# Kernel optimization log

Hardware: AMD Instinct MI355X
Metric: run time of the kernel (lower is better)

The kernel has to match this reference:

```python
import jax, jax.numpy as jnp
import numpy as np

MARGIN = 0.1
LAMBDA_EFFECT = 0.5

B, T_V, K, T_S = 32, 8192, 64, 128


def setup_inputs() -> dict:
    key = jax.random.key(0)
    k1, k2, k3, k4, k5 = jax.random.split(key, 5)
    pred_orig = jax.random.normal(k1, (B, T_V), dtype=jnp.float32)
    pred_intervened = jax.random.normal(k2, (K, B, T_V), dtype=jnp.float32)
    intervened_indices = jax.random.randint(k3, (K,), 0, T_S, dtype=jnp.int32)
    # GT alignment mask: sparse-ish binary alignment between frames and sentences
    gt_mask = jax.random.bernoulli(k4, 0.2, (B, T_V, T_S)).astype(jnp.int32)
    # prefix-valid video mask: valid length per batch in [T_V//2, T_V]
    lengths = jax.random.randint(k5, (B,), T_V // 2, T_V + 1, dtype=jnp.int32)
    mask_video = (jnp.arange(T_V, dtype=jnp.int32)[None, :] < lengths[:, None]).astype(jnp.int32)
    return {
        "pred_orig": pred_orig,
        "pred_intervened": pred_intervened,
        "intervened_indices": intervened_indices,
        "gt_mask": gt_mask,
        "mask_video": mask_video,
    }


def reference(pred_orig, pred_intervened, intervened_indices, gt_mask, mask_video):
    # pred_orig: [B,T], pred_intervened: [K,B,T], gt_mask: [B,T,S], mask_video: [B,T]
    prob_orig = jax.nn.sigmoid(pred_orig)                 # [B,T]
    prob_int = jax.nn.sigmoid(pred_intervened)            # [K,B,T]
    effect = jnp.abs(prob_orig[None, :, :] - prob_int)    # [K,B,T]

    valid = mask_video.astype(bool)                       # [B,T] (prefix mask == :T_v_valid slice)
    # gather intervened sentence columns: [B,T,K] -> [K,B,T]
    gt_sel = jnp.transpose(gt_mask[:, :, intervened_indices], (2, 0, 1))

    aligned = (gt_sel > 0) & valid[None]                  # [K,B,T]
    non_aligned = (gt_sel == 0) & valid[None]             # [K,B,T]

    cnt_a = aligned.sum(axis=-1)                          # [K,B]
    cnt_n = non_aligned.sum(axis=-1)                      # [K,B]

    ea = jnp.sum(effect * aligned, axis=-1) / jnp.maximum(cnt_a, 1)
    en = jnp.sum(effect * non_aligned, axis=-1) / jnp.maximum(cnt_n, 1)

    per_pair = jnp.where((cnt_a > 0) & (cnt_n > 0),
                         jax.nn.relu(MARGIN - (ea - en)),
                         jnp.zeros_like(ea))
    num_interventions = pred_orig.shape[0] * pred_intervened.shape[0]
    alignment_consistency = per_pair.sum() / max(num_interventions, 1)
    total_intervention_loss = alignment_consistency * LAMBDA_EFFECT
    return alignment_consistency, total_intervention_loss
```

## Files before the change

### kernel.cpp

```cpp
#include <hip/hip_runtime.h>
#include <cstdint>

#define BB 32
#define TV 8192
#define KK 64
#define TS 128
#define MARGIN_F 0.1f
#define LAMBDA_F 0.5f

static constexpr size_t WSA_OFF = 0;
static constexpr size_t WSV_OFF = (size_t)BB * TV * 8;
static constexpr size_t ACC_OFF = WSV_OFF + (size_t)BB * (TV / 64) * 8;

__global__ __launch_bounds__(256) void pack_kernel(
    const int* __restrict__ gt, const int* __restrict__ mv,
    const int* __restrict__ idx,
    unsigned long long* __restrict__ wsA, unsigned long long* __restrict__ wsV) {
  const int lane = threadIdx.x & 63;
  const int wave = blockIdx.x * 4 + (threadIdx.x >> 6);
  const int r0 = wave * 64;
  const int c = idx[lane];
  const int csel = c & 3, csh = c >> 2;

  const unsigned long long V = __ballot(mv[r0 + lane] != 0);
  if (lane == 0) wsV[r0 >> 6] = V;

  const int4* rowp = (const int4*)(gt + (size_t)r0 * TS);
#pragma unroll 2
  for (int ch = 0; ch < 32; ++ch) {
    int4 v = rowp[ch * 64 + lane];
    unsigned long long b0 = __ballot(v.x > 0);
    unsigned long long b1 = __ballot(v.y > 0);
    unsigned long long b2 = __ballot(v.z > 0);
    unsigned long long b3 = __ballot(v.w > 0);
    unsigned long long sel = (csel == 0) ? b0 : (csel == 1) ? b1 : (csel == 2) ? b2 : b3;
    int raw0 = (int)((sel >> csh) & 1ull);
    int raw1 = (int)((sel >> (32 + csh)) & 1ull);
    const int rlo = 2 * ch, rhi = 2 * ch + 1;
    const int v0 = (int)((V >> rlo) & 1ull);
    const int v1 = (int)((V >> rhi) & 1ull);
    unsigned long long A0 = __ballot(v0 & raw0);
    unsigned long long A1 = __ballot(v1 & raw1);
    if (lane == 0) {
      wsA[r0 + rlo] = A0;
      wsA[r0 + rhi] = A1;
    }
  }
}

__global__ __launch_bounds__(256) void main_kernel(
    const float* __restrict__ po, const float* __restrict__ pi,
    const unsigned long long* __restrict__ wsA,
    const unsigned long long* __restrict__ wsV, float* __restrict__ acc) {
  const int k = blockIdx.x & (KK - 1);
  const int b = blockIdx.x >> 6;
  const float* pik = pi + ((size_t)k * BB + b) * TV;
  const float* pob = po + (size_t)b * TV;
  const unsigned long long* Ab = wsA + (size_t)b * TV;
  const unsigned long long* Vb = wsV + (size_t)b * (TV / 64);

  float ea = 0.f, en = 0.f;
  int ca = 0, cn = 0;
  for (int t = threadIdx.x; t < TV; t += 256) {
    const float xo = pob[t];
    const float xi = pik[t];
    const unsigned long long A = Ab[t];
    const int valid = (int)((Vb[t >> 6] >> (t & 63)) & 1ull);
    const int ab = (int)((A >> k) & 1ull);
    const int nb = valid & (ab ^ 1);
    const float so = 1.f / (1.f + __expf(-xo));
    const float si = 1.f / (1.f + __expf(-xi));
    const float eff = fabsf(so - si);
    ea += ab ? eff : 0.f;
    en += nb ? eff : 0.f;
    ca += ab;
    cn += nb;
  }
#pragma unroll
  for (int off = 32; off > 0; off >>= 1) {
    ea += __shfl_down(ea, off);
    en += __shfl_down(en, off);
    ca += __shfl_down(ca, off);
    cn += __shfl_down(cn, off);
  }
  __shared__ float sea[4], sen[4];
  __shared__ int sca[4], scn[4];
  const int w = threadIdx.x >> 6;
  if ((threadIdx.x & 63) == 0) { sea[w] = ea; sen[w] = en; sca[w] = ca; scn[w] = cn; }
  __syncthreads();
  if (threadIdx.x == 0) {
    float EA = 0.f, EN = 0.f;
    int CA = 0, CN = 0;
#pragma unroll
    for (int i = 0; i < 4; ++i) { EA += sea[i]; EN += sen[i]; CA += sca[i]; CN += scn[i]; }
    float pp = 0.f;
    if (CA > 0 && CN > 0) {
      const float d = MARGIN_F - (EA / (float)CA - EN / (float)CN);
      pp = d > 0.f ? d : 0.f;
    }
    atomicAdd(acc, pp);
  }
}

__global__ void fin_kernel(const float* __restrict__ acc, float* __restrict__ out) {
  const float s = acc[0] * (1.0f / (float)(BB * KK));
  out[0] = s;
  out[1] = s * LAMBDA_F;
}

extern "C" void kernel_launch(void* const* d_in, const int* in_sizes, int n_in,
                              void* d_out, int out_size, void* d_ws, size_t ws_size,
                              hipStream_t stream) {
  const float* pred_orig = (const float*)d_in[0];
  const float* pred_int  = (const float*)d_in[1];
  const int*   idx       = (const int*)d_in[2];
  const int*   gt        = (const int*)d_in[3];
  const int*   mv        = (const int*)d_in[4];
  float* out = (float*)d_out;

  char* ws = (char*)d_ws;
  unsigned long long* wsA = (unsigned long long*)(ws + WSA_OFF);
  unsigned long long* wsV = (unsigned long long*)(ws + WSV_OFF);
  float* acc = (float*)(ws + ACC_OFF);

  hipMemsetAsync(acc, 0, sizeof(float), stream);
  pack_kernel<<<1024, 256, 0, stream>>>(gt, mv, idx, wsA, wsV);
  main_kernel<<<BB * KK, 256, 0, stream>>>(pred_orig, pred_int, wsA, wsV, acc);
  fin_kernel<<<1, 1, 0, stream>>>(acc, out);
}
```

Baseline: 280.0 us.

## Fuse mask packing and effect reduction into one row-tiled kernel with atomics

Merges the pack and main kernels so each wave packs the aligned bits for its 64 rows into LDS, then loops over all K interventions for those rows. The per-row workspace bitmask no longer makes a round trip through global memory, pred_orig sigmoid is computed once per row instead of K times, and one launch is removed. Non-aligned sums are derived as valid-minus-aligned in a small final kernel. The cost is many float atomics (three per wave per k, plus one per wave for the valid count) and strided access to pred_intervened across k.

```diff
diff --git a/kernel.cpp b/kernel.cpp
--- a/kernel.cpp
+++ b/kernel.cpp
@@ -8,22 +8,27 @@
 #define MARGIN_F 0.1f
 #define LAMBDA_F 0.5f
 
-static constexpr size_t WSA_OFF = 0;
-static constexpr size_t WSV_OFF = (size_t)BB * TV * 8;
-static constexpr size_t ACC_OFF = WSV_OFF + (size_t)BB * (TV / 64) * 8;
+static constexpr int KSTR = BB * TV;
 
-__global__ __launch_bounds__(256) void pack_kernel(
-    const int* __restrict__ gt, const int* __restrict__ mv,
-    const int* __restrict__ idx,
-    unsigned long long* __restrict__ wsA, unsigned long long* __restrict__ wsV) {
+
+__global__ __launch_bounds__(256) void fused_kernel(
+    const float* __restrict__ po, const float* __restrict__ pi,
+    const int* __restrict__ idx, const int* __restrict__ gt,
+    const int* __restrict__ mv,
+    float* __restrict__ gsa, float* __restrict__ gsv,
+    float* __restrict__ gca, float* __restrict__ gcv) {
   const int lane = threadIdx.x & 63;
-  const int wave = blockIdx.x * 4 + (threadIdx.x >> 6);
+  const int w = threadIdx.x >> 6;
+  const int wave = blockIdx.x * 4 + w;
   const int r0 = wave * 64;
+  const int b = r0 >> 13;
   const int c = idx[lane];
   const int csel = c & 3, csh = c >> 2;
 
+  __shared__ unsigned long long lA[256];
+  unsigned long long* A = lA + w * 64;
+
   const unsigned long long V = __ballot(mv[r0 + lane] != 0);
-  if (lane == 0) wsV[r0 >> 6] = V;
 
   const int4* rowp = (const int4*)(gt + (size_t)r0 * TS);
 #pragma unroll 2
@@ -41,71 +46,67 @@
     const int v1 = (int)((V >> rhi) & 1ull);
     unsigned long long A0 = __ballot(v0 & raw0);
     unsigned long long A1 = __ballot(v1 & raw1);
+    if (lane == 0) { A[rlo] = A0; A[rhi] = A1; }
+  }
+  __syncthreads();
+
+  const unsigned long long Am = A[lane];
+  const int vb = (int)((V >> lane) & 1ull);
+  const float xo = po[r0 + lane];
+  const float so = 1.f / (1.f + __expf(-xo));
+  const float* pik = pi + r0 + lane;
+
+  if (lane == 0) atomicAdd(&gcv[b], (float)__popcll(V));
+
+#pragma unroll 4
+  for (int k = 0; k < KK; ++k) {
+    const float xi = pik[(size_t)k * KSTR];
+    const float si = 1.f / (1.f + __expf(-xi));
+    const float eff = fabsf(so - si);
+    const int ab = (int)((Am >> k) & 1ull);
+    float sa = ab ? eff : 0.f;
+    float sv = vb ? eff : 0.f;
+#pragma unroll
+    for (int off = 32; off > 0; off >>= 1) {
+      sa += __shfl_down(sa, off);
+      sv += __shfl_down(sv, off);
+    }
+    const unsigned long long cab = __ballot(ab != 0);
     if (lane == 0) {
-      wsA[r0 + rlo] = A0;
-      wsA[r0 + rhi] = A1;
+      atomicAdd(&gsa[k * BB + b], sa);
+      atomicAdd(&gsv[k * BB + b], sv);
+      atomicAdd(&gca[k * BB + b], (float)__popcll(cab));
     }
   }
 }
 
-__global__ __launch_bounds__(256) void main_kernel(
-    const float* __restrict__ po, const float* __restrict__ pi,
-    const unsigned long long* __restrict__ wsA,
-    const unsigned long long* __restrict__ wsV, float* __restrict__ acc) {
-  const int k = blockIdx.x & (KK - 1);
-  const int b = blockIdx.x >> 6;
-  const float* pik = pi + ((size_t)k * BB + b) * TV;
-  const float* pob = po + (size_t)b * TV;
-  const unsigned long long* Ab = wsA + (size_t)b * TV;
-  const unsigned long long* Vb = wsV + (size_t)b * (TV / 64);
-
-  float ea = 0.f, en = 0.f;
-  int ca = 0, cn = 0;
-  for (int t = threadIdx.x; t < TV; t += 256) {
-    const float xo = pob[t];
-    const float xi = pik[t];
-    const unsigned long long A = Ab[t];
-    const int valid = (int)((Vb[t >> 6] >> (t & 63)) & 1ull);
-    const int ab = (int)((A >> k) & 1ull);
-    const int nb = valid & (ab ^ 1);
-    const float so = 1.f / (1.f + __expf(-xo));
-    const float si = 1.f / (1.f + __expf(-xi));
-    const float eff = fabsf(so - si);
-    ea += ab ? eff : 0.f;
-    en += nb ? eff : 0.f;
-    ca += ab;
-    cn += nb;
+__global__ __launch_bounds__(256) void fin_kernel(
+    const float* __restrict__ gsa, const float* __restrict__ gsv,
+    const float* __restrict__ gca, const float* __restrict__ gcv,
+    float* __restrict__ out) {
+  float s = 0.f;
+  for (int i = threadIdx.x; i < KK * BB; i += 256) {
+    const int b = i & (BB - 1);
+    const float ca = gca[i];
+    const float cn = gcv[b] - ca;
+    if (ca > 0.f && cn > 0.f) {
+      const float sa = gsa[i];
+      const float sv = gsv[i];
+      const float d = MARGIN_F - (sa / ca - (sv - sa) / cn);
+      s += d > 0.f ? d : 0.f;
+    }
   }
 #pragma unroll
-  for (int off = 32; off > 0; off >>= 1) {
-    ea += __shfl_down(ea, off);
-    en += __shfl_down(en, off);
-    ca += __shfl_down(ca, off);
-    cn += __shfl_down(cn, off);
-  }
-  __shared__ float sea[4], sen[4];
-  __shared__ int sca[4], scn[4];
-  const int w = threadIdx.x >> 6;
-  if ((threadIdx.x & 63) == 0) { sea[w] = ea; sen[w] = en; sca[w] = ca; scn[w] = cn; }
+  for (int off = 32; off > 0; off >>= 1) s += __shfl_down(s, off);
+  __shared__ float ws4[4];
+  if ((threadIdx.x & 63) == 0) ws4[threadIdx.x >> 6] = s;
   __syncthreads();
   if (threadIdx.x == 0) {
-    float EA = 0.f, EN = 0.f;
-    int CA = 0, CN = 0;
-#pragma unroll
-    for (int i = 0; i < 4; ++i) { EA += sea[i]; EN += sen[i]; CA += sca[i]; CN += scn[i]; }
-    float pp = 0.f;
-    if (CA > 0 && CN > 0) {
-      const float d = MARGIN_F - (EA / (float)CA - EN / (float)CN);
-      pp = d > 0.f ? d : 0.f;
-    }
-    atomicAdd(acc, pp);
+    const float S = ws4[0] + ws4[1] + ws4[2] + ws4[3];
+    const float ac = S * (1.0f / (float)(KK * BB));
+    out[0] = ac;
+    out[1] = ac * LAMBDA_F;
   }
-}
-
-__global__ void fin_kernel(const float* __restrict__ acc, float* __restrict__ out) {
-  const float s = acc[0] * (1.0f / (float)(BB * KK));
-  out[0] = s;
-  out[1] = s * LAMBDA_F;
 }
 
 extern "C" void kernel_launch(void* const* d_in, const int* in_sizes, int n_in,
@@ -118,13 +119,13 @@
   const int*   mv        = (const int*)d_in[4];
   float* out = (float*)d_out;
 
-  char* ws = (char*)d_ws;
-  unsigned long long* wsA = (unsigned long long*)(ws + WSA_OFF);
-  unsigned long long* wsV = (unsigned long long*)(ws + WSV_OFF);
-  float* acc = (float*)(ws + ACC_OFF);
+  float* gsa = (float*)d_ws;
+  float* gsv = gsa + KK * BB;
+  float* gca = gsv + KK * BB;
+  float* gcv = gca + KK * BB;
 
-  hipMemsetAsync(acc, 0, sizeof(float), stream);
-  pack_kernel<<<1024, 256, 0, stream>>>(gt, mv, idx, wsA, wsV);
-  main_kernel<<<BB * KK, 256, 0, stream>>>(pred_orig, pred_int, wsA, wsV, acc);
-  fin_kernel<<<1, 1, 0, stream>>>(acc, out);
+  hipMemsetAsync(d_ws, 0, (size_t)(3 * KK * BB + BB) * sizeof(float), stream);
+  fused_kernel<<<(BB * TV) / (64 * 4), 256, 0, stream>>>(
+      pred_orig, pred_int, idx, gt, mv, gsa, gsv, gca, gcv);
+  fin_kernel<<<1, 256, 0, stream>>>(gsa, gsv, gca, gcv, out);
 }
```

New measurement: 397.9 us. 42.1% more time.

## Transpose alignment bitplanes, skip invalid tail, vectorize main loop with derived counts

Applied to the files above, without the earlier changes.

The pack kernel now builds per-lane bitplanes, one 64-bit word per (frame-block, intervention), with fewer ballots and stores. It also skips gt reads for fully invalid frame blocks and counts valid lengths with atomics. The main kernel stages the masks for its (b,k) in shared memory and loads float4 vectors. It stops at the valid length rounded up to 1024, which avoids reading the masked tail of pred_intervened. The non-aligned sum and count are derived from the valid-total minus the aligned part, which costs an extra atomic pass in pack and depends on the mask being a prefix.

```diff
diff --git a/kernel.cpp b/kernel.cpp
--- a/kernel.cpp
+++ b/kernel.cpp
@@ -8,94 +8,124 @@
 #define MARGIN_F 0.1f
 #define LAMBDA_F 0.5f
 
-static constexpr size_t WSA_OFF = 0;
-static constexpr size_t WSV_OFF = (size_t)BB * TV * 8;
-static constexpr size_t ACC_OFF = WSV_OFF + (size_t)BB * (TV / 64) * 8;
+static constexpr int KSTR = BB * TV;
+static constexpr int WPB = TV / 64;
+static constexpr int NWAVE = BB * WPB;
+
+static constexpr size_t ACC_OFF = 0;
+static constexpr size_t LEN_OFF = 64;
+static constexpr size_t WSV_OFF = 4096;
+static constexpr size_t WSA_OFF = 65536;
 
 __global__ __launch_bounds__(256) void pack_kernel(
     const int* __restrict__ gt, const int* __restrict__ mv,
     const int* __restrict__ idx,
-    unsigned long long* __restrict__ wsA, unsigned long long* __restrict__ wsV) {
+    unsigned long long* __restrict__ wsA, unsigned long long* __restrict__ wsV,
+    int* __restrict__ len) {
   const int lane = threadIdx.x & 63;
   const int wave = blockIdx.x * 4 + (threadIdx.x >> 6);
   const int r0 = wave * 64;
+  const int b = r0 >> 13;
   const int c = idx[lane];
   const int csel = c & 3, csh = c >> 2;
 
   const unsigned long long V = __ballot(mv[r0 + lane] != 0);
-  if (lane == 0) wsV[r0 >> 6] = V;
+  if (lane == 0) {
+    wsV[wave] = V;
+    atomicAdd(&len[b], __popcll(V));
+  }
 
-  const int4* rowp = (const int4*)(gt + (size_t)r0 * TS);
-#pragma unroll 2
-  for (int ch = 0; ch < 32; ++ch) {
-    int4 v = rowp[ch * 64 + lane];
-    unsigned long long b0 = __ballot(v.x > 0);
-    unsigned long long b1 = __ballot(v.y > 0);
-    unsigned long long b2 = __ballot(v.z > 0);
-    unsigned long long b3 = __ballot(v.w > 0);
-    unsigned long long sel = (csel == 0) ? b0 : (csel == 1) ? b1 : (csel == 2) ? b2 : b3;
-    int raw0 = (int)((sel >> csh) & 1ull);
-    int raw1 = (int)((sel >> (32 + csh)) & 1ull);
-    const int rlo = 2 * ch, rhi = 2 * ch + 1;
-    const int v0 = (int)((V >> rlo) & 1ull);
-    const int v1 = (int)((V >> rhi) & 1ull);
-    unsigned long long A0 = __ballot(v0 & raw0);
-    unsigned long long A1 = __ballot(v1 & raw1);
-    if (lane == 0) {
-      wsA[r0 + rlo] = A0;
-      wsA[r0 + rhi] = A1;
+  unsigned long long plane = 0ull;
+  if (V != 0ull) {
+    const int4* rowp = (const int4*)(gt + (size_t)r0 * TS);
+#pragma unroll 4
+    for (int ch = 0; ch < 32; ++ch) {
+      int4 v = rowp[ch * 64 + lane];
+      unsigned long long b0 = __ballot(v.x > 0);
+      unsigned long long b1 = __ballot(v.y > 0);
+      unsigned long long b2 = __ballot(v.z > 0);
+      unsigned long long b3 = __ballot(v.w > 0);
+      unsigned long long sel =
+          (csel == 0) ? b0 : (csel == 1) ? b1 : (csel == 2) ? b2 : b3;
+      const unsigned long long raw0 = (sel >> csh) & 1ull;
+      const unsigned long long raw1 = (sel >> (32 + csh)) & 1ull;
+      plane |= (raw0 << (2 * ch)) | (raw1 << (2 * ch + 1));
     }
+    plane &= V;
   }
+  wsA[(size_t)wave * 64 + lane] = plane;
 }
 
 __global__ __launch_bounds__(256) void main_kernel(
     const float* __restrict__ po, const float* __restrict__ pi,
     const unsigned long long* __restrict__ wsA,
-    const unsigned long long* __restrict__ wsV, float* __restrict__ acc) {
+    const unsigned long long* __restrict__ wsV,
+    const int* __restrict__ len, float* __restrict__ acc) {
   const int k = blockIdx.x & (KK - 1);
   const int b = blockIdx.x >> 6;
-  const float* pik = pi + ((size_t)k * BB + b) * TV;
+  const int tid = threadIdx.x;
+
+  __shared__ unsigned long long sA[WPB];
+  __shared__ unsigned long long sV[WPB];
+  if (tid < WPB) sA[tid] = wsA[(size_t)(b * WPB + tid) * 64 + k];
+  else           sV[tid - WPB] = wsV[b * WPB + (tid - WPB)];
+  __syncthreads();
+
   const float* pob = po + (size_t)b * TV;
-  const unsigned long long* Ab = wsA + (size_t)b * TV;
-  const unsigned long long* Vb = wsV + (size_t)b * (TV / 64);
+  const float* pik = pi + (size_t)k * KSTR + (size_t)b * TV;
+  const int L = len[b];
+  const int Tlim = (L + 1023) & ~1023;
 
-  float ea = 0.f, en = 0.f;
-  int ca = 0, cn = 0;
-  for (int t = threadIdx.x; t < TV; t += 256) {
-    const float xo = pob[t];
-    const float xi = pik[t];
-    const unsigned long long A = Ab[t];
-    const int valid = (int)((Vb[t >> 6] >> (t & 63)) & 1ull);
-    const int ab = (int)((A >> k) & 1ull);
-    const int nb = valid & (ab ^ 1);
-    const float so = 1.f / (1.f + __expf(-xo));
-    const float si = 1.f / (1.f + __expf(-xi));
-    const float eff = fabsf(so - si);
-    ea += ab ? eff : 0.f;
-    en += nb ? eff : 0.f;
-    ca += ab;
-    cn += nb;
+  float sa = 0.f, sv = 0.f;
+  int ca = 0;
+  for (int t0 = tid * 4; t0 < Tlim; t0 += 1024) {
+    const float4 xo = *(const float4*)(pob + t0);
+    const float4 xi = *(const float4*)(pik + t0);
+    const int sh = t0 & 63;
+    const unsigned ab = (unsigned)((sA[t0 >> 6] >> sh) & 15ull);
+    const unsigned vb = (unsigned)((sV[t0 >> 6] >> sh) & 15ull);
+    {
+      const float e = fabsf(1.f / (1.f + __expf(-xo.x)) - 1.f / (1.f + __expf(-xi.x)));
+      if (ab & 1u) sa += e;
+      if (vb & 1u) sv += e;
+    }
+    {
+      const float e = fabsf(1.f / (1.f + __expf(-xo.y)) - 1.f / (1.f + __expf(-xi.y)));
+      if (ab & 2u) sa += e;
+      if (vb & 2u) sv += e;
+    }
+    {
+      const float e = fabsf(1.f / (1.f + __expf(-xo.z)) - 1.f / (1.f + __expf(-xi.z)));
+      if (ab & 4u) sa += e;
+      if (vb & 4u) sv += e;
+    }
+    {
+      const float e = fabsf(1.f / (1.f + __expf(-xo.w)) - 1.f / (1.f + __expf(-xi.w)));
+      if (ab & 8u) sa += e;
+      if (vb & 8u) sv += e;
+    }
+    ca += __popc(ab);
   }
+
+  float fca = (float)ca;
 #pragma unroll
   for (int off = 32; off > 0; off >>= 1) {
-    ea += __shfl_down(ea, off);
-    en += __shfl_down(en, off);
-    ca += __shfl_down(ca, off);
-    cn += __shfl_down(cn, off);
+    sa += __shfl_down(sa, off);
+    sv += __shfl_down(sv, off);
+    fca += __shfl_down(fca, off);
   }
-  __shared__ float sea[4], sen[4];
-  __shared__ int sca[4], scn[4];
-  const int w = threadIdx.x >> 6;
-  if ((threadIdx.x & 63) == 0) { sea[w] = ea; sen[w] = en; sca[w] = ca; scn[w] = cn; }
+  __shared__ float p0[4], p1[4], p2[4];
+  const int w = tid >> 6;
+  if ((tid & 63) == 0) { p0[w] = sa; p1[w] = sv; p2[w] = fca; }
   __syncthreads();
-  if (threadIdx.x == 0) {
-    float EA = 0.f, EN = 0.f;
-    int CA = 0, CN = 0;
-#pragma unroll
-    for (int i = 0; i < 4; ++i) { EA += sea[i]; EN += sen[i]; CA += sca[i]; CN += scn[i]; }
+  if (tid == 0) {
+    const float SA = p0[0] + p0[1] + p0[2] + p0[3];
+    const float SV = p1[0] + p1[1] + p1[2] + p1[3];
+    const float CA = p2[0] + p2[1] + p2[2] + p2[3];
+    const float CN = (float)L - CA;
     float pp = 0.f;
-    if (CA > 0 && CN > 0) {
-      const float d = MARGIN_F - (EA / (float)CA - EN / (float)CN);
+    if (CA > 0.f && CN > 0.f) {
+      const float d = MARGIN_F - (SA / CA - (SV - SA) / CN);
       pp = d > 0.f ? d : 0.f;
     }
     atomicAdd(acc, pp);
@@ -103,9 +133,9 @@
 }
 
 __global__ void fin_kernel(const float* __restrict__ acc, float* __restrict__ out) {
-  const float s = acc[0] * (1.0f / (float)(BB * KK));
-  out[0] = s;
-  out[1] = s * LAMBDA_F;
+  const float ac = acc[0] * (1.0f / (float)(KK * BB));
+  out[0] = ac;
+  out[1] = ac * LAMBDA_F;
 }
 
 extern "C" void kernel_launch(void* const* d_in, const int* in_sizes, int n_in,
@@ -119,12 +149,13 @@
   float* out = (float*)d_out;
 
   char* ws = (char*)d_ws;
+  float* acc = (float*)(ws + ACC_OFF);
+  int* len = (int*)(ws + LEN_OFF);
+  unsigned long long* wsV = (unsigned long long*)(ws + WSV_OFF);
   unsigned long long* wsA = (unsigned long long*)(ws + WSA_OFF);
-  unsigned long long* wsV = (unsigned long long*)(ws + WSV_OFF);
-  float* acc = (float*)(ws + ACC_OFF);
 
-  hipMemsetAsync(acc, 0, sizeof(float), stream);
-  pack_kernel<<<1024, 256, 0, stream>>>(gt, mv, idx, wsA, wsV);
-  main_kernel<<<BB * KK, 256, 0, stream>>>(pred_orig, pred_int, wsA, wsV, acc);
+  hipMemsetAsync(ws, 0, 192, stream);
+  pack_kernel<<<NWAVE / 4, 256, 0, stream>>>(gt, mv, idx, wsA, wsV, len);
+  main_kernel<<<BB * KK, 256, 0, stream>>>(pred_orig, pred_int, wsA, wsV, len, acc);
   fin_kernel<<<1, 1, 0, stream>>>(acc, out);
 }
```

Measured after the change: 292.9 us. +4.6%, slower.
